# Kernel tuning notes

Measured on AMD Instinct MI355X. Metric: run time of the kernel, lower is better.

The kernel has to match this reference:

```python
import jax, jax.numpy as jnp
import numpy as np

HEAD_DIM = 128
NUM_Q_HEADS = 16
NUM_KV_HEADS = 8
EPS = 1e-6


def _rope_tables(seq_len, head_dim, base=10000.0):
    inv_freq = 1.0 / (base ** (np.arange(0, head_dim, 2, dtype=np.float32) / head_dim))
    t = np.arange(seq_len, dtype=np.float32)
    freqs = np.outer(t, inv_freq)                      # [S, hd/2]
    emb = np.concatenate([freqs, freqs], axis=-1)      # [S, hd]
    return jnp.asarray(np.cos(emb)), jnp.asarray(np.sin(emb))


def setup_inputs() -> dict:
    key = jax.random.key(0)
    k1, k2, k3 = jax.random.split(key, 3)
    B, S, D = 2, 2048, 2048
    qo_dim = NUM_Q_HEADS * HEAD_DIM
    kv_dim = NUM_KV_HEADS * HEAD_DIM
    x = jax.random.normal(k1, (B, S, D), dtype=jnp.float32)
    w_qkv = jax.random.normal(k2, (qo_dim + 2 * kv_dim, D), dtype=jnp.float32) * 0.02
    w_o = jax.random.normal(k3, (D, qo_dim), dtype=jnp.float32) * 0.02
    pos_cos, pos_sin = _rope_tables(S, HEAD_DIM)
    return {
        "x": x,
        "pos_cos": pos_cos,
        "pos_sin": pos_sin,
        "w_qkv": w_qkv,
        "w_o": w_o,
        "q_norm_w": jnp.ones((HEAD_DIM,), dtype=jnp.float32),
        "k_norm_w": jnp.ones((HEAD_DIM,), dtype=jnp.float32),
    }


def _rms_norm(h, w):
    # per-head RMSNorm over last dim (head_dim)
    var = jnp.mean(jnp.square(h), axis=-1, keepdims=True)
    return h * jax.lax.rsqrt(var + EPS) * w


def _rotate_half(h):
    h1, h2 = jnp.split(h, 2, axis=-1)
    return jnp.concatenate([-h2, h1], axis=-1)


def _apply_rope(h, cos, sin):
    # h: [B, S, H, hd]; cos/sin: [S, hd]
    c = cos[None, :, None, :]
    s = sin[None, :, None, :]
    return h * c + _rotate_half(h) * s


def reference(x, pos_cos, pos_sin, w_qkv, w_o, q_norm_w, k_norm_w):
    B, S, D = x.shape
    hd = HEAD_DIM
    qkv = jnp.einsum("bsd,ed->bse", x, w_qkv).reshape(B, S, -1, hd)
    q = qkv[:, :, :NUM_Q_HEADS]                                   # [B,S,Hq,hd]
    k = qkv[:, :, NUM_Q_HEADS:NUM_Q_HEADS + NUM_KV_HEADS]         # [B,S,Hk,hd]
    v = qkv[:, :, NUM_Q_HEADS + NUM_KV_HEADS:]                    # [B,S,Hk,hd]

    q = _apply_rope(_rms_norm(q, q_norm_w), pos_cos, pos_sin)
    k = _apply_rope(_rms_norm(k, k_norm_w), pos_cos, pos_sin)

    # GQA: expand kv heads to match query heads
    rep = NUM_Q_HEADS // NUM_KV_HEADS
    k = jnp.repeat(k, rep, axis=2)
    v = jnp.repeat(v, rep, axis=2)

    scale = 1.0 / jnp.sqrt(jnp.float32(hd))
    scores = jnp.einsum("bqhd,bkhd->bhqk", q, k) * scale          # [B,H,S,S]
    causal = jnp.tril(jnp.ones((S, S), dtype=bool))
    scores = jnp.where(causal[None, None], scores, jnp.finfo(scores.dtype).min)
    attn = jax.nn.softmax(scores, axis=-1)
    out = jnp.einsum("bhqk,bkhd->bqhd", attn, v)                  # [B,S,H,hd]
    out = out.reshape(B, S, NUM_Q_HEADS * hd)
    return jnp.einsum("bse,de->bsd", out, w_o)
```

## Files before the change

### kernel.cpp

```cpp
#include <hip/hip_runtime.h>
#include <hip/hip_bf16.h>
#include <stdint.h>

#define HD 128
#define NQH 16
#define NKVH 8
#define SEQ 2048
#define DMODEL 2048
#define BATCH 2

typedef __attribute__((ext_vector_type(8))) short bf16x8;
typedef __attribute__((ext_vector_type(4))) float f32x4;
typedef __attribute__((ext_vector_type(16))) float f32x16;

__device__ __forceinline__ ushort f2bf(float f){
  union { float f; uint32_t u; } v; v.f = f;
  uint32_t u = v.u;
  return (ushort)((u + 0x7FFFu + ((u >> 16) & 1u)) >> 16);
}
__device__ __forceinline__ float bf2f(ushort h){
  union { uint32_t u; float f; } v; v.u = ((uint32_t)h) << 16; return v.f;
}
__device__ __forceinline__ void gload16(const void* g, void* l){
  __builtin_amdgcn_global_load_lds((const __attribute__((address_space(1))) void*)g,
                                   (__attribute__((address_space(3))) void*)l, 16, 0, 0);
}
__device__ __forceinline__ unsigned int cvtpk(float lo, float hi){
  unsigned int r;
  asm("v_cvt_pk_bf16_f32 %0, %1, %2" : "=v"(r) : "v"(lo), "v"(hi));
  return r;
}

__global__ void cvtbf(const float* __restrict__ in, ushort* __restrict__ out, int n4){
  int i = blockIdx.x * 256 + threadIdx.x;
  if (i < n4){
    float4 v = ((const float4*)in)[i];
    ushort4 o;
    o.x = f2bf(v.x); o.y = f2bf(v.y); o.z = f2bf(v.z); o.w = f2bf(v.w);
    ((ushort4*)out)[i] = o;
  }
}

template<int OUTF32>
__global__ __launch_bounds__(256) void gemm_bt(const ushort* __restrict__ A,
                                               const ushort* __restrict__ B,
                                               void* __restrict__ C,
                                               int M, int N, int K){
  __shared__ __align__(16) ushort lA[128*64];
  __shared__ __align__(16) ushort lB[128*64];
  const int tid = threadIdx.x;
  const int l = tid & 63, w = tid >> 6;
  const int m0 = blockIdx.y * 128, n0 = blockIdx.x * 128;
  const int wr = (w >> 1) * 64, wc = (w & 1) * 64;
  f32x4 acc[4][4];
  #pragma unroll
  for (int m=0;m<4;m++)
    #pragma unroll
    for (int n=0;n<4;n++) acc[m][n] = f32x4{0.f,0.f,0.f,0.f};

  const int srow = l >> 3;
  const int scol = ((l & 7) ^ srow) << 3;
  const ushort* gA = A + (size_t)(m0 + w*32 + srow) * K + scol;
  const ushort* gB = B + (size_t)(n0 + w*32 + srow) * K + scol;
  ushort* lAw = &lA[(w*32) * 64];
  ushort* lBw = &lB[(w*32) * 64];

  for (int kt = 0; kt < K; kt += 64){
    __syncthreads();
    #pragma unroll
    for (int j=0;j<4;j++){
      gload16(gA + kt + (size_t)(j*8)*K, lAw + j*8*64);
      gload16(gB + kt + (size_t)(j*8)*K, lBw + j*8*64);
    }
    __syncthreads();
    #pragma unroll
    for (int kk=0; kk<2; kk++){
      bf16x8 af[4], bb[4];
      #pragma unroll
      for (int m=0;m<4;m++){
        int row = wr + m*16 + (l & 15);
        int slot = (kk*4 + (l >> 4)) ^ (row & 7);
        af[m] = *(const bf16x8*)&lA[row*64 + slot*8];
      }
      #pragma unroll
      for (int n=0;n<4;n++){
        int row = wc + n*16 + (l & 15);
        int slot = (kk*4 + (l >> 4)) ^ (row & 7);
        bb[n] = *(const bf16x8*)&lB[row*64 + slot*8];
      }
      #pragma unroll
      for (int m=0;m<4;m++)
        #pragma unroll
        for (int n=0;n<4;n++)
          acc[m][n] = __builtin_amdgcn_mfma_f32_16x16x32_bf16(af[m], bb[n], acc[m][n], 0,0,0);
    }
  }
  #pragma unroll
  for (int m=0;m<4;m++)
    #pragma unroll
    for (int n=0;n<4;n++)
      #pragma unroll
      for (int r=0;r<4;r++){
        size_t row = (size_t)(m0 + wr + m*16 + (l>>4)*4 + r);
        size_t col = (size_t)(n0 + wc + n*16 + (l & 15));
        float v = acc[m][n][r];
        if (OUTF32) ((float*)C)[row*N + col] = v;
        else        ((ushort*)C)[row*N + col] = f2bf(v);
      }
}

__global__ __launch_bounds__(256) void norm_rope(const ushort* __restrict__ qkv,
                                                 const float* __restrict__ cosT,
                                                 const float* __restrict__ sinT,
                                                 const float* __restrict__ qw,
                                                 const float* __restrict__ kw,
                                                 ushort* __restrict__ Qo,
                                                 ushort* __restrict__ Ko){
  int gw = (blockIdx.x * 256 + threadIdx.x) >> 6;
  int l = threadIdx.x & 63;
  int head = gw % 24;
  int bs = gw / 24;
  int s = bs & (SEQ-1);
  int b = bs >> 11;
  ushort2 hv = *(const ushort2*)(qkv + (size_t)bs*(2*DMODEL) + head*HD + l*2);
  float h0 = bf2f(hv.x), h1 = bf2f(hv.y);
  float ss = h0*h0 + h1*h1;
  #pragma unroll
  for (int m=1; m<64; m<<=1) ss += __shfl_xor(ss, m);
  float rinv = rsqrtf(ss * (1.0f/128.0f) + 1e-6f);
  const float* wp = (head < NQH) ? qw : kw;
  float w0 = wp[l*2], w1 = wp[l*2+1];
  float n0 = h0 * rinv * w0, n1 = h1 * rinv * w1;
  float p0 = __shfl_xor(n0, 32), p1 = __shfl_xor(n1, 32);
  float r0 = (l < 32) ? -p0 : p0;
  float r1 = (l < 32) ? -p1 : p1;
  float c0 = cosT[s*HD + l*2], c1 = cosT[s*HD + l*2 + 1];
  float s0 = sinT[s*HD + l*2], s1 = sinT[s*HD + l*2 + 1];
  float sc = (head < NQH) ? 0.12751656062f : 1.0f;
  ushort2 o;
  o.x = f2bf((n0*c0 + r0*s0) * sc);
  o.y = f2bf((n1*c1 + r1*s1) * sc);
  if (head < NQH)
    *(ushort2*)(Qo + ((size_t)((b*NQH + head)*SEQ) + s)*HD + l*2) = o;
  else
    *(ushort2*)(Ko + ((size_t)((b*NKVH + (head-NQH))*SEQ) + s)*HD + l*2) = o;
}

__global__ __launch_bounds__(256) void vtrans(const ushort* __restrict__ qkv, ushort* __restrict__ vt){
  __shared__ __align__(16) ushort t[64][136];
  int bid = blockIdx.x;
  int st = bid & 31, kh = (bid >> 5) & 7, b = bid >> 8;
  int s0 = st * 64;
  int tid = threadIdx.x;
  #pragma unroll
  for (int it=0; it<4; it++){
    int row = (tid >> 4) + it*16;
    int c = tid & 15;
    uint4 v = *(const uint4*)&qkv[((size_t)(b*SEQ + s0 + row))*(2*DMODEL) + (NQH+NKVH+kh)*HD + c*8];
    *(uint4*)&t[row][c*8] = v;
  }
  __syncthreads();
  #pragma unroll
  for (int it=0; it<4; it++){
    int g = it*256 + tid;
    int d = g >> 3, c = g & 7;
    ushort tmp[8] __attribute__((aligned(16)));
    #pragma unroll
    for (int j=0;j<8;j++) tmp[j] = t[c*8+j][d];
    *(uint4*)&vt[((size_t)((b*NKVH+kh)*HD + d))*SEQ + s0 + c*8] = *(uint4*)tmp;
  }
}

__global__ __launch_bounds__(256, 2) void attn_fwd(const ushort* __restrict__ Q,
                                                   const ushort* __restrict__ Kb,
                                                   const ushort* __restrict__ Vt,
                                                   ushort* __restrict__ O){
  __shared__ __align__(16) ushort lK[2][64*128];
  __shared__ __align__(16) ushort lV[2][128*64];
  const int l = threadIdx.x & 63, w = threadIdx.x >> 6;
  const int wq = w >> 1, wkv = w & 1;
  const int hl = l >> 5, q32 = l & 31;
  const int e = blockIdx.x, head = blockIdx.y, b = blockIdx.z;
  const int kh = head >> 1;

  const ushort* kg = Kb + (size_t)((b*NKVH + kh)*SEQ) * HD;
  const ushort* vg = Vt + (size_t)((b*NKVH + kh)*HD) * SEQ;

  auto STAGE = [&](int t, int bi){
    const int kv0 = t*64;
    #pragma unroll
    for (int j=0;j<4;j++){
      int krow = kv0 + w*16 + j*4 + (l>>4);
      gload16(kg + (size_t)krow*HD + (((l&15) ^ (krow&15))<<3),
              &lK[bi][(w*16 + j*4)*128]);
      int vrow = w*32 + j*8 + (l>>3);
      gload16(vg + (size_t)vrow*SEQ + kv0 + (((l&7) ^ (l>>3))<<3),
              &lV[bi][(w*32 + j*8)*64]);
    }
  };

  auto run_tile = [&](int qt){
    const int qb = qt*64 + wq*32;
    const ushort* qp = Q + ((size_t)((b*NQH + head)*SEQ) + qb + q32) * HD + hl*8;
    bf16x8 qf[8];
    #pragma unroll
    for (int ks=0; ks<8; ks++) qf[ks] = *(const bf16x8*)(qp + ks*16);

    float mrun = -1e30f, lrun = 0.f;
    f32x16 acc[4];
    #pragma unroll
    for (int dt=0;dt<4;dt++)
      #pragma unroll
      for (int r=0;r<16;r++) acc[dt][r] = 0.f;

    STAGE(0, 0);
    __syncthreads();

    for (int t=0; t<=qt; t++){
      if (t < qt) STAGE(t+1, (t+1)&1);
      const int bi = t & 1;
      const bool skip = (t==qt) && (wq==0) && (wkv==1);
      if (!skip){
        f32x16 s;
        #pragma unroll
        for (int r=0;r<16;r++) s[r] = 0.f;
        const int rowT = wkv*32 + q32;
        #pragma unroll
        for (int ks=0; ks<8; ks++){
          int slot = (ks*2 + hl) ^ (rowT & 15);
          bf16x8 kf = *(const bf16x8*)&lK[bi][rowT*128 + slot*8];
          s = __builtin_amdgcn_mfma_f32_32x32x16_bf16(kf, qf[ks], s, 0,0,0);
        }
        if (t==qt && wq==wkv){
          const int qg = qb + q32;
          #pragma unroll
          for (int r=0;r<16;r++){
            int kvg = t*64 + wkv*32 + (r&3) + 8*(r>>2) + 4*hl;
            s[r] = (kvg > qg) ? -1e30f : s[r];
          }
        }
        float t0 = fmaxf(fmaxf(s[0],s[1]),fmaxf(s[2],s[3]));
        float t1 = fmaxf(fmaxf(s[4],s[5]),fmaxf(s[6],s[7]));
        float t2 = fmaxf(fmaxf(s[8],s[9]),fmaxf(s[10],s[11]));
        float t3 = fmaxf(fmaxf(s[12],s[13]),fmaxf(s[14],s[15]));
        float tmax = fmaxf(fmaxf(t0,t1),fmaxf(t2,t3));
        tmax = fmaxf(tmax, __shfl_xor(tmax, 32));
        if (!__all(tmax <= mrun)){
          float mnew = fmaxf(mrun, tmax);
          float corr = __builtin_amdgcn_exp2f(mrun - mnew);
          mrun = mnew; lrun *= corr;
          #pragma unroll
          for (int r=0;r<16;r++){
            int qr = (r&3) + 8*(r>>2) + 4*hl;
            float cr = __shfl(corr, qr);
            acc[0][r]*=cr; acc[1][r]*=cr; acc[2][r]*=cr; acc[3][r]*=cr;
          }
        }
        #pragma unroll
        for (int r=0;r<16;r++) s[r] = __builtin_amdgcn_exp2f(s[r] - mrun);
        float r0s = (s[0]+s[1])+(s[2]+s[3]);
        float r1s = (s[4]+s[5])+(s[6]+s[7]);
        float r2s = (s[8]+s[9])+(s[10]+s[11]);
        float r3s = (s[12]+s[13])+(s[14]+s[15]);
        float rs = (r0s+r1s)+(r2s+r3s);
        rs += __shfl_xor(rs, 32);
        lrun += rs;
        #pragma unroll
        for (int ks2=0; ks2<2; ks2++){
          unsigned int A = cvtpk(s[8*ks2+0], s[8*ks2+1]);
          unsigned int B = cvtpk(s[8*ks2+2], s[8*ks2+3]);
          unsigned int C = cvtpk(s[8*ks2+4], s[8*ks2+5]);
          unsigned int D = cvtpk(s[8*ks2+6], s[8*ks2+7]);
          auto sw0 = __builtin_amdgcn_permlane32_swap(A, C, false, false);
          auto sw1 = __builtin_amdgcn_permlane32_swap(B, D, false, false);
          union { unsigned int u[4]; bf16x8 v; } pw;
          pw.u[0]=sw0[0]; pw.u[1]=sw1[0]; pw.u[2]=sw0[1]; pw.u[3]=sw1[1];
          #pragma unroll
          for (int dt=0; dt<4; dt++){
            int d = dt*32 + q32;
            int slot = (wkv*4 + ks2*2 + hl) ^ (d & 7);
            bf16x8 vf = *(const bf16x8*)&lV[bi][d*64 + slot*8];
            acc[dt] = __builtin_amdgcn_mfma_f32_32x32x16_bf16(pw.v, vf, acc[dt], 0,0,0);
          }
        }
      }
      __syncthreads();
    }

    float* mergeO = (float*)(&lK[0][0]) + wq*4096;
    float* mergeML = (float*)(&lV[0][0]);
    if (wkv == 1){
      #pragma unroll
      for (int dt=0; dt<4; dt++)
        #pragma unroll
        for (int rg=0; rg<4; rg++){
          f32x4 o = { acc[dt][rg*4+0], acc[dt][rg*4+1], acc[dt][rg*4+2], acc[dt][rg*4+3] };
          *(f32x4*)&mergeO[(dt*4+rg)*256 + l*4] = o;
        }
      if (l < 32){
        mergeML[wq*64 + l] = mrun;
        mergeML[wq*64 + 32 + l] = lrun;
      }
    }
    __syncthreads();
    if (wkv == 0){
      float m1 = mergeML[wq*64 + q32];
      float l1 = mergeML[wq*64 + 32 + q32];
      float mf = fmaxf(mrun, m1);
      float c0 = __builtin_amdgcn_exp2f(mrun - mf);
      float c1 = __builtin_amdgcn_exp2f(m1 - mf);
      float lt = lrun*c0 + l1*c1;
      float linv = 1.0f / lt;
      float f0 = c0 * linv, f1 = c1 * linv;
      float g0a[16], g1a[16];
      #pragma unroll
      for (int r=0;r<16;r++){
        int qr = (r&3) + 8*(r>>2) + 4*hl;
        g0a[r] = __shfl(f0, qr);
        g1a[r] = __shfl(f1, qr);
      }
      #pragma unroll
      for (int dt=0; dt<4; dt++)
        #pragma unroll
        for (int rg=0; rg<4; rg++){
          f32x4 o1 = *(const f32x4*)&mergeO[(dt*4+rg)*256 + l*4];
          #pragma unroll
          for (int j=0;j<4;j++){
            int r = rg*4 + j;
            int qr = (r&3) + 8*(r>>2) + 4*hl;
            float val = acc[dt][r]*g0a[r] + o1[j]*g1a[r];
            int orow = qt*64 + wq*32 + qr;
            O[((size_t)(b*SEQ) + orow)*DMODEL + head*HD + dt*32 + q32] = f2bf(val);
          }
        }
    }
    __syncthreads();
  };

  run_tile(e);
  run_tile(31 - e);
}

extern "C" void kernel_launch(void* const* d_in, const int* in_sizes, int n_in,
                              void* d_out, int out_size, void* d_ws, size_t ws_size,
                              hipStream_t stream){
  const float* x    = (const float*)d_in[0];
  const float* pcos = (const float*)d_in[1];
  const float* psin = (const float*)d_in[2];
  const float* wqkv = (const float*)d_in[3];
  const float* wo   = (const float*)d_in[4];
  const float* qnw  = (const float*)d_in[5];
  const float* knw  = (const float*)d_in[6];
  char* ws = (char*)d_ws;

  ushort* xb    = (ushort*)(ws + 0);
  ushort* wqkvb = (ushort*)(ws + 16777216);
  ushort* wob   = (ushort*)(ws + 33554432);
  ushort* qkv   = (ushort*)(ws + 41943040);
  ushort* qbuf  = (ushort*)(ws + 75497472);
  ushort* kbuf  = (ushort*)(ws + 92274688);
  ushort* vtb   = (ushort*)(ws + 100663296);
  ushort* aout  = (ushort*)(ws + 0);

  cvtbf<<<8192, 256, 0, stream>>>(x,    xb,    2097152);
  cvtbf<<<8192, 256, 0, stream>>>(wqkv, wqkvb, 2097152);
  cvtbf<<<4096, 256, 0, stream>>>(wo,   wob,   1048576);

  gemm_bt<0><<<dim3(32,32), 256, 0, stream>>>(xb, wqkvb, qkv, 4096, 4096, 2048);

  norm_rope<<<24576, 256, 0, stream>>>(qkv, pcos, psin, qnw, knw, qbuf, kbuf);
  vtrans<<<512, 256, 0, stream>>>(qkv, vtb);

  attn_fwd<<<dim3(16,16,2), 256, 0, stream>>>(qbuf, kbuf, vtb, aout);

  gemm_bt<1><<<dim3(16,32), 256, 0, stream>>>(aout, wob, d_out, 4096, 2048, 2048);
}
```

Baseline: 241.2 us.

## Add 256x256-tile pipelined GEMM kernel for the QKV projection

Adds a new 512-thread GEMM kernel with 256x256 output tiles, double-buffered LDS staging through global_load_lds, XOR-swizzled LDS layout, and loads for upcoming K tiles interleaved between the four MFMA phases. It replaces the 128x128-tile gemm_bt for the QKV projection. The larger tiles raise data reuse and cut global traffic per FLOP, and the interleaving overlaps memory with compute. In exchange it allows only one block per CU, makes just 256 blocks, and relies on hand-placed waitcnt and barrier choices whose correctness is tied to load ordering.

Measured after the change: 224.1 us. 7.1% less time.

```diff
diff --git a/kernel.cpp b/kernel.cpp
--- a/kernel.cpp
+++ b/kernel.cpp
@@ -106,6 +106,107 @@
         float v = acc[m][n][r];
         if (OUTF32) ((float*)C)[row*N + col] = v;
         else        ((ushort*)C)[row*N + col] = f2bf(v);
+      }
+}
+
+__global__ __launch_bounds__(512, 1) void gemm256_bt(const ushort* __restrict__ A,
+                                                     const ushort* __restrict__ B,
+                                                     ushort* __restrict__ C,
+                                                     int M, int N, int K){
+  __shared__ __align__(16) ushort lA[2][256*64];
+  __shared__ __align__(16) ushort lB[2][256*64];
+  const int tid = threadIdx.x;
+  const int l = tid & 63, w = tid >> 6;
+  const int wm = w >> 2, wn = w & 3;
+  const int m0 = blockIdx.y * 256, n0 = blockIdx.x * 256;
+  const int NT = K >> 6;
+
+  const int srow = w*8 + (l >> 3);
+  const int scol = ((l & 7) ^ (l >> 3)) << 3;
+
+  f32x4 acc[8][4];
+  #pragma unroll
+  for (int m=0;m<8;m++)
+    #pragma unroll
+    for (int n=0;n<4;n++) acc[m][n] = f32x4{0.f,0.f,0.f,0.f};
+
+  auto stgA = [&](int t, int h){
+    const int bi = t & 1;
+    #pragma unroll
+    for (int j=0;j<2;j++)
+      gload16(A + (size_t)(m0 + h*128 + j*64 + srow)*K + t*64 + scol,
+              &lA[bi][(h*128 + j*64 + w*8)*64]);
+  };
+  auto stgB = [&](int t, int h){
+    const int bi = t & 1;
+    #pragma unroll
+    for (int j=0;j<2;j++)
+      gload16(B + (size_t)(n0 + h*128 + j*64 + srow)*K + t*64 + scol,
+              &lB[bi][(h*128 + j*64 + w*8)*64]);
+  };
+
+  stgA(0,0); stgA(0,1); stgB(0,0); stgB(0,1);
+  stgA(1,0); stgB(1,0); stgB(1,1);
+  asm volatile("s_waitcnt vmcnt(6)" ::: "memory");
+  __builtin_amdgcn_s_barrier();
+
+  for (int t=0; t<NT; t++){
+    const int bi = t & 1;
+    bf16x8 bfr[4][2];
+    #pragma unroll
+    for (int q=0; q<4; q++){
+      bf16x8 af[2][2];
+      #pragma unroll
+      for (int mi2=0; mi2<2; mi2++)
+        #pragma unroll
+        for (int ks=0; ks<2; ks++){
+          int row = wm*128 + (q*2 + mi2)*16 + (l & 15);
+          int slot = (ks*4 + (l >> 4)) ^ (l & 7);
+          af[mi2][ks] = *(const bf16x8*)&lA[bi][row*64 + slot*8];
+        }
+      if (q == 0){
+        #pragma unroll
+        for (int ni=0; ni<4; ni++)
+          #pragma unroll
+          for (int ks=0; ks<2; ks++){
+            int row = wn*64 + ni*16 + (l & 15);
+            int slot = (ks*4 + (l >> 4)) ^ (l & 7);
+            bfr[ni][ks] = *(const bf16x8*)&lB[bi][row*64 + slot*8];
+          }
+      }
+      if (q == 0 && t+1 < NT) stgA(t+1, 1);
+      if (q == 1 && t+2 < NT) stgB(t+2, 0);
+      if (q == 2 && t+2 < NT) stgB(t+2, 1);
+      __builtin_amdgcn_s_barrier();
+      asm volatile("s_waitcnt lgkmcnt(0)" ::: "memory");
+      if (q == 3 && t+2 < NT) stgA(t+2, 0);
+      __builtin_amdgcn_s_setprio(1);
+      #pragma unroll
+      for (int mi2=0; mi2<2; mi2++)
+        #pragma unroll
+        for (int ni=0; ni<4; ni++)
+          #pragma unroll
+          for (int ks=0; ks<2; ks++)
+            acc[q*2+mi2][ni] = __builtin_amdgcn_mfma_f32_16x16x32_bf16(
+                af[mi2][ks], bfr[ni][ks], acc[q*2+mi2][ni], 0,0,0);
+      __builtin_amdgcn_s_setprio(0);
+      if (q == 3){
+        if (t < NT-2) { asm volatile("s_waitcnt vmcnt(6)" ::: "memory"); }
+        else          { asm volatile("s_waitcnt vmcnt(0)" ::: "memory"); }
+      }
+      __builtin_amdgcn_s_barrier();
+    }
+  }
+
+  #pragma unroll
+  for (int mi=0; mi<8; mi++)
+    #pragma unroll
+    for (int ni=0; ni<4; ni++)
+      #pragma unroll
+      for (int r=0; r<4; r++){
+        size_t row = (size_t)(m0 + wm*128 + mi*16 + (l>>4)*4 + r);
+        size_t col = (size_t)(n0 + wn*64 + ni*16 + (l & 15));
+        C[row*N + col] = f2bf(acc[mi][ni][r]);
       }
 }
 
@@ -366,7 +467,7 @@
   cvtbf<<<8192, 256, 0, stream>>>(wqkv, wqkvb, 2097152);
   cvtbf<<<4096, 256, 0, stream>>>(wo,   wob,   1048576);
 
-  gemm_bt<0><<<dim3(32,32), 256, 0, stream>>>(xb, wqkvb, qkv, 4096, 4096, 2048);
+  gemm256_bt<<<dim3(16,16), 512, 0, stream>>>(xb, wqkvb, qkv, 4096, 4096, 2048);
 
   norm_rope<<<24576, 256, 0, stream>>>(qkv, pcos, psin, qnw, knw, qbuf, kbuf);
   vtrans<<<512, 256, 0, stream>>>(qkv, vtb);
```
